# Kernel optimization log

Measured on AMD Instinct MI355X. Metric: run time of the kernel, lower is better.

Reference implementation:

```python
import jax, jax.numpy as jnp
import numpy as np

NEG_SLOPE = 0.2  # PyG GATConv default negative_slope


def _segment_softmax(alpha, dst, n):
    m = jax.ops.segment_max(alpha, dst, num_segments=n)
    m = jnp.where(jnp.isfinite(m), m, 0.0)
    ex = jnp.exp(alpha - m[dst])
    den = jax.ops.segment_sum(ex, dst, num_segments=n)
    return ex / (den[dst] + 1e-16)


def _gat_layer(x, src, dst, eattr, W, att_src, att_dst, We, att_e, b, n):
    h = x @ W                                        # [N, C]
    a = (h @ att_src)[src] + (h @ att_dst)[dst] + (eattr @ We) @ att_e  # [E]
    a = jax.nn.leaky_relu(a, NEG_SLOPE)
    coef = _segment_softmax(a, dst, n)               # edge-wise attention
    out = jax.ops.segment_sum(coef[:, None] * h[src], dst, num_segments=n)
    return out + b


def _glorot(key, shape):
    fan_in, fan_out = shape[0], shape[-1]
    s = jnp.sqrt(6.0 / (fan_in + fan_out))
    return jax.random.uniform(key, shape, jnp.float32, -s, s)


def setup_inputs() -> dict:
    N, E, D, ED = 100000, 1600000, 128, 16
    key = jax.random.key(0)
    ks = jax.random.split(key, 32)
    inp = {
        'x': jax.random.normal(ks[0], (N, D), jnp.float32),
        'edge_index': jax.random.randint(ks[1], (2, E), 0, N, jnp.int64),
        'edge_attr': jax.random.normal(ks[2], (E, ED), jnp.float32),
    }
    dims = [(D, 64), (64, 32), (32, 16)]
    i = 3
    for li, (din, dout) in enumerate(dims, 1):
        inp[f'W{li}'] = _glorot(ks[i], (din, dout)); i += 1
        inp[f'att_src{li}'] = _glorot(ks[i], (dout,)); i += 1
        inp[f'att_dst{li}'] = _glorot(ks[i], (dout,)); i += 1
        inp[f'We{li}'] = _glorot(ks[i], (ED, dout)); i += 1
        inp[f'att_e{li}'] = _glorot(ks[i], (dout,)); i += 1
        inp[f'b{li}'] = jnp.zeros((dout,), jnp.float32)
    return inp


def reference(x, edge_index, edge_attr,
              W1, att_src1, att_dst1, We1, att_e1, b1,
              W2, att_src2, att_dst2, We2, att_e2, b2,
              W3, att_src3, att_dst3, We3, att_e3, b3):
    n = x.shape[0]
    src, dst = edge_index[0], edge_index[1]
    # add self-loops; self-loop edge_attr = mean of incoming edge attrs (fill_value='mean')
    cnt = jax.ops.segment_sum(jnp.ones_like(dst, dtype=edge_attr.dtype), dst, num_segments=n)
    loop_attr = jax.ops.segment_sum(edge_attr, dst, num_segments=n) / jnp.maximum(cnt, 1.0)[:, None]
    loops = jnp.arange(n, dtype=src.dtype)
    src2 = jnp.concatenate([src, loops])
    dst2 = jnp.concatenate([dst, loops])
    ea2 = jnp.concatenate([edge_attr, loop_attr], axis=0)

    h = jax.nn.elu(_gat_layer(x, src2, dst2, ea2, W1, att_src1, att_dst1, We1, att_e1, b1, n))
    h = jax.nn.elu(_gat_layer(h, src2, dst2, ea2, W2, att_src2, att_dst2, We2, att_e2, b2, n))
    z = _gat_layer(h, src2, dst2, ea2, W3, att_src3, att_dst3, We3, att_e3, b3, n)
    return z
```

## Files before the change

### kernel.cpp

```cpp
#include <hip/hip_runtime.h>
#include <hip/hip_bf16.h>

typedef __hip_bfloat16 bf16;

__device__ __forceinline__ float lrelu(float a) { return a > 0.f ? a : 0.2f * a; }
__device__ __forceinline__ int clampi(int v, int hi) { return v < 0 ? 0 : (v >= hi ? hi - 1 : v); }
__device__ __forceinline__ float ldx(const void* p, size_t i, int f32) {
  return f32 ? ((const float*)p)[i] : (float)((const bf16*)p)[i];
}
__device__ __forceinline__ float4 ldx4(const void* p, size_t i, int f32) {
  if (f32) return *(const float4*)((const float*)p + i);
  const __hip_bfloat162* q = (const __hip_bfloat162*)((const bf16*)p + i);
  float2 a = __bfloat1622float2(q[0]), b = __bfloat1622float2(q[1]);
  return make_float4(a.x, a.y, b.x, b.y);
}

__device__ __forceinline__ void edge_qs(const void* eattr, size_t e, int f32, const float* w,
                                        float& q1, float& q2, float& q3) {
  float v[16];
  if (f32) {
    const float4* p = (const float4*)((const float*)eattr + e * 16);
#pragma unroll
    for (int j = 0; j < 4; ++j) {
      float4 t = p[j];
      v[4 * j] = t.x; v[4 * j + 1] = t.y; v[4 * j + 2] = t.z; v[4 * j + 3] = t.w;
    }
  } else {
    const __hip_bfloat162* p = (const __hip_bfloat162*)((const bf16*)eattr + e * 16);
#pragma unroll
    for (int j = 0; j < 8; ++j) {
      float2 t = __bfloat1622float2(p[j]);
      v[2 * j] = t.x; v[2 * j + 1] = t.y;
    }
  }
  q1 = 0.f; q2 = 0.f; q3 = 0.f;
#pragma unroll
  for (int j = 0; j < 16; ++j) {
    q1 += v[j] * w[j];
    q2 += v[j] * w[16 + j];
    q3 += v[j] * w[32 + j];
  }
}

__global__ __launch_bounds__(256) void detwv_k(const int* __restrict__ ei32,
                                               const unsigned short* __restrict__ xw, int E,
                                               int* __restrict__ flags, const void* We1,
                                               const void* ae1, const void* We2, const void* ae2,
                                               const void* We3, const void* ae3,
                                               float* __restrict__ wv) {
  __shared__ int s64, sf;
  int t = threadIdx.x;
  if (t == 0) { s64 = 1; sf = 0; }
  __syncthreads();
  int lim = E < 2048 ? E : 2048;
  for (int k = t; k < lim; k += 256)
    if (ei32[2 * k + 1] != 0) atomicAnd(&s64, 0);
  int hit = 0;
  for (int k = t; k < 4096; k += 256) {
    int ex = (xw[k] >> 7) & 0xFF;
    if (ex >= 0xC3) hit = 1;
  }
  if (hit) atomicOr(&sf, 1);
  __syncthreads();
  if (t == 0) { flags[0] = s64; flags[1] = sf; }
  int f32 = sf;
  if (t < 48) {
    int l = t >> 4, j = t & 15;
    const void* We = l == 0 ? We1 : (l == 1 ? We2 : We3);
    const void* ae = l == 0 ? ae1 : (l == 1 ? ae2 : ae3);
    int Cc = l == 0 ? 64 : (l == 1 ? 32 : 16);
    float s = 0.f;
    for (int c = 0; c < Cc; ++c) s += ldx(We, (size_t)j * Cc + c, f32) * ldx(ae, c, f32);
    wv[l * 16 + j] = s;
  }
}

__global__ __launch_bounds__(256) void count_k(const int* __restrict__ ei32, int E, int N,
                                               const int* __restrict__ flags,
                                               int* __restrict__ cnt, int* __restrict__ rank) {
  int e = blockIdx.x * 256 + threadIdx.x;
  if (e >= E) return;
  int is64 = flags[0] != 0;
  int d = is64 ? ei32[2 * ((size_t)E + e)] : ei32[(size_t)E + e];
  rank[e] = atomicAdd(&cnt[clampi(d, N)], 1);
}

__global__ __launch_bounds__(1024) void scan1_k(const int* __restrict__ cnt, int* __restrict__ excl,
                                                int* __restrict__ bsum, int n) {
  __shared__ int sh[1024];
  int i = blockIdx.x * 1024 + threadIdx.x;
  int v = (i < n) ? cnt[i] : 0;
  sh[threadIdx.x] = v;
  __syncthreads();
  for (int off = 1; off < 1024; off <<= 1) {
    int t = (threadIdx.x >= off) ? sh[threadIdx.x - off] : 0;
    __syncthreads();
    sh[threadIdx.x] += t;
    __syncthreads();
  }
  if (i < n) excl[i] = sh[threadIdx.x] - v;
  if (threadIdx.x == 1023) bsum[blockIdx.x] = sh[1023];
}

__global__ __launch_bounds__(128) void scan2_k(int* bsum, int nb) {
  __shared__ int sh[128];
  int t = threadIdx.x;
  int v = (t < nb) ? bsum[t] : 0;
  sh[t] = v;
  __syncthreads();
  for (int off = 1; off < 128; off <<= 1) {
    int x = (t >= off) ? sh[t - off] : 0;
    __syncthreads();
    sh[t] += x;
    __syncthreads();
  }
  if (t < nb) bsum[t] = sh[t] - v;
}

template <bool FOLD>
__global__ __launch_bounds__(256) void scan3_k(int* __restrict__ row_ptr,
                                               const int* __restrict__ bsum, int n, int E,
                                               int nb) {
  __shared__ int pref[128];
  int t = threadIdx.x;
  if (FOLD) {
    if (t < 128) pref[t] = (t < nb) ? bsum[t] : 0;
    __syncthreads();
    for (int off = 1; off < 128; off <<= 1) {
      int x = 0;
      if (t < 128 && t >= off) x = pref[t - off];
      __syncthreads();
      if (t < 128) pref[t] += x;
      __syncthreads();
    }
  }
  int i = blockIdx.x * 256 + t;
  if (i < n) {
    int blk = i >> 10;
    int add = FOLD ? (blk == 0 ? 0 : pref[blk - 1]) : bsum[blk];
    row_ptr[i] = row_ptr[i] + add;
  }
  if (i == 0) row_ptr[n] = E;
}

__global__ __launch_bounds__(256) void scatter_k(const int* __restrict__ ei32, const void* eattr,
                                                 const float* __restrict__ wv,
                                                 const int* __restrict__ flags,
                                                 const int* __restrict__ row_ptr,
                                                 const int* __restrict__ rank,
                                                 float4* __restrict__ recs, int E, int N) {
  __shared__ float w[48];
  if (threadIdx.x < 48) w[threadIdx.x] = wv[threadIdx.x];
  __syncthreads();
  int e = blockIdx.x * 256 + threadIdx.x;
  if (e >= E) return;
  int is64 = flags[0] != 0, f32 = flags[1] != 0;
  int s = is64 ? ei32[2 * (size_t)e] : ei32[e];
  int d = is64 ? ei32[2 * ((size_t)E + e)] : ei32[(size_t)E + e];
  s = clampi(s, N);
  d = clampi(d, N);
  int rk = rank[e];
  int base = row_ptr[d];
  float q1, q2, q3;
  edge_qs(eattr, (size_t)e, f32, w, q1, q2, q3);
  recs[clampi(base + rk, E)] = make_float4(__int_as_float(s), q1, q2, q3);
}

template <int K, int C, bool XEXT>
__global__ __launch_bounds__(256, 4) void mm3_k(const void* Xv, const void* Wv, const void* ats_v,
                                                const void* atd_v, const int* __restrict__ flags,
                                                int N, float* __restrict__ h,
                                                float* __restrict__ as_, float* __restrict__ ad_) {
  static_assert(K == 2 * C, "");
  constexpr int NCG = C / 8;
  constexpr int TM = 512 / NCG;
  __shared__ __align__(16) float Wl[K * C];
  __shared__ __align__(16) float Xl[32 * TM];
  const int f32 = flags[1];
  const int tid = threadIdx.x;
  for (int i = tid; i < K * C; i += 256) Wl[i] = ldx(Wv, i, f32);
  const int cg = tid & (NCG - 1);
  const int ng = tid / NCG;
  const int c0 = cg * 8;
  float ats[8], atd[8];
#pragma unroll
  for (int j = 0; j < 8; ++j) {
    ats[j] = ldx(ats_v, c0 + j, f32);
    atd[j] = ldx(atd_v, c0 + j, f32);
  }
  const int n_base = blockIdx.x * TM;
  float acc[2][8];
#pragma unroll
  for (int i = 0; i < 2; ++i)
#pragma unroll
    for (int j = 0; j < 8; ++j) acc[i][j] = 0.f;

#pragma unroll 1
  for (int kc = 0; kc < K / 32; ++kc) {
    __syncthreads();
#pragma unroll
    for (int t = 0; t < TM / 32; ++t) {
      int f = tid + t * 256;
      int node = f >> 3, kq = f & 7;
      int gn = n_base + node;
      if (gn >= N) gn = N - 1;
      float4 v;
      if (XEXT)
        v = ldx4(Xv, (size_t)gn * K + kc * 32 + kq * 4, f32);
      else
        v = *(const float4*)((const float*)Xv + (size_t)gn * K + kc * 32 + kq * 4);
      int col = node ^ (kq * 4);
      Xl[(kq * 4 + 0) * TM + col] = v.x;
      Xl[(kq * 4 + 1) * TM + col] = v.y;
      Xl[(kq * 4 + 2) * TM + col] = v.z;
      Xl[(kq * 4 + 3) * TM + col] = v.w;
    }
    __syncthreads();
#pragma unroll 8
    for (int kk = 0; kk < 32; ++kk) {
      const float2 xv = *(const float2*)&Xl[kk * TM + ((2 * ng) ^ ((kk >> 2) * 4))];
      const float4 w0 = *(const float4*)&Wl[(kc * 32 + kk) * C + c0];
      const float4 w1 = *(const float4*)&Wl[(kc * 32 + kk) * C + c0 + 4];
      const float ws[8] = {w0.x, w0.y, w0.z, w0.w, w1.x, w1.y, w1.z, w1.w};
#pragma unroll
      for (int j = 0; j < 8; ++j) {
        acc[0][j] += xv.x * ws[j];
        acc[1][j] += xv.y * ws[j];
      }
    }
  }
#pragma unroll
  for (int i = 0; i < 2; ++i) {
    int n = n_base + ng * 2 + i;
    float vs = 0.f, vd = 0.f;
#pragma unroll
    for (int j = 0; j < 8; ++j) {
      vs += acc[i][j] * ats[j];
      vd += acc[i][j] * atd[j];
    }
#pragma unroll
    for (int off = NCG / 2; off > 0; off >>= 1) {
      vs += __shfl_xor(vs, off, NCG);
      vd += __shfl_xor(vd, off, NCG);
    }
    if (n < N) {
      float* hr = &h[(size_t)n * C + c0];
      *(float4*)hr = make_float4(acc[i][0], acc[i][1], acc[i][2], acc[i][3]);
      *(float4*)(hr + 4) = make_float4(acc[i][4], acc[i][5], acc[i][6], acc[i][7]);
      if (cg == 0) {
        as_[n] = vs;
        ad_[n] = vd;
      }
    }
  }
}

template <int C, int QC, bool ELU, bool LAST>
__global__ __launch_bounds__(256) void agg_k(const int* __restrict__ row_ptr,
                                             const float4* __restrict__ recs,
                                             const float* __restrict__ as_,
                                             const float* __restrict__ ad_,
                                             const float* __restrict__ h, const void* b,
                                             const int* __restrict__ flags, void* out, int N,
                                             int E) {
  const int GR = 256 / C;
  constexpr int LP = C / 4;
  const float SHIFT = 10.0f;
  __shared__ int ss[256];
  __shared__ float sp[256];
  int lane = threadIdx.x & (C - 1);
  int grp = threadIdx.x / C;
  int slot0 = grp * C;
  int qtr = lane / LP;
  int lh = lane % LP;
  int f32 = flags[1];
  float bc = ldx(b, lane, f32);
  for (int n = blockIdx.x * GR + grp; n < N; n += gridDim.x * GR) {
    int start = row_ptr[n], end = row_ptr[n + 1];
    int deg = end > start ? end - start : 0;
    float adn = ad_[n];
    float denl = 0.f, qacc = 0.f;
    float4 a4 = make_float4(0.f, 0.f, 0.f, 0.f);
    for (int base = 0; base < deg; base += C) {
      int cnt = deg - base < C ? deg - base : C;
      int sj = 0;
      float pj = 0.f, qv = 0.f;
      if (lane < cnt) {
        float4 r = recs[start + base + lane];
        sj = clampi(__float_as_int(r.x), N);
        qv = ((const float*)&r)[QC];
        float aj = lrelu(as_[sj] + adn + qv);
        pj = __expf(aj - SHIFT);
      }
      qacc += qv;
      denl += pj;
      ss[slot0 + lane] = sj;
      sp[slot0 + lane] = pj;
      float4 s4 = make_float4(0.f, 0.f, 0.f, 0.f);
      int nt = (cnt + 3) >> 2;
#pragma unroll 4
      for (int t = 0; t < nt; ++t) {
        int r = t * 4 + qtr;
        int s = ss[slot0 + r];
        float p = sp[slot0 + r];
        const float4 hv = *(const float4*)&h[(size_t)s * C + 4 * lh];
        s4.x += p * hv.x;
        s4.y += p * hv.y;
        s4.z += p * hv.z;
        s4.w += p * hv.w;
      }
      a4.x += s4.x;
      a4.y += s4.y;
      a4.z += s4.z;
      a4.w += s4.w;
    }
    float den = denl, qsum = qacc;
#pragma unroll
    for (int off = C / 2; off > 0; off >>= 1) {
      den += __shfl_xor(den, off, C);
      qsum += __shfl_xor(qsum, off, C);
    }
    a4.x += __shfl_xor(a4.x, LP, C);
    a4.y += __shfl_xor(a4.y, LP, C);
    a4.z += __shfl_xor(a4.z, LP, C);
    a4.w += __shfl_xor(a4.w, LP, C);
    a4.x += __shfl_xor(a4.x, 2 * LP, C);
    a4.y += __shfl_xor(a4.y, 2 * LP, C);
    a4.z += __shfl_xor(a4.z, 2 * LP, C);
    a4.w += __shfl_xor(a4.w, 2 * LP, C);
    int ml = lane >> 2, bsel = lane & 3;
    float vx = __shfl(a4.x, ml, C);
    float vy = __shfl(a4.y, ml, C);
    float vz = __shfl(a4.z, ml, C);
    float vw = __shfl(a4.w, ml, C);
    float acc = bsel == 0 ? vx : (bsel == 1 ? vy : (bsel == 2 ? vz : vw));
    float qloop = qsum / fmaxf((float)deg, 1.0f);
    float aself = lrelu(as_[n] + adn + qloop);
    float pself = __expf(aself - SHIFT);
    den += pself;
    acc += pself * h[(size_t)n * C + lane];
    float o = acc / den + bc;
    if (ELU) o = o > 0.f ? o : (__expf(o) - 1.0f);
    if (LAST && !f32)
      ((bf16*)out)[(size_t)n * C + lane] = (bf16)o;
    else
      ((float*)out)[(size_t)n * C + lane] = o;
  }
}

extern "C" void kernel_launch(void* const* d_in, const int* in_sizes, int n_in, void* d_out,
                              int out_size, void* d_ws, size_t ws_size, hipStream_t stream) {
  const void* x = d_in[0];
  const int* ei32 = (const int*)d_in[1];
  void* eattr = d_in[2];
  const void *W1 = d_in[3], *s1 = d_in[4], *t1 = d_in[5], *We1 = d_in[6], *ae1 = d_in[7],
             *b1 = d_in[8];
  const void *W2 = d_in[9], *s2 = d_in[10], *t2 = d_in[11], *We2 = d_in[12], *ae2 = d_in[13],
             *b2 = d_in[14];
  const void *W3 = d_in[15], *s3 = d_in[16], *t3 = d_in[17], *We3 = d_in[18], *ae3 = d_in[19],
             *b3 = d_in[20];

  const int N = in_sizes[0] / 128;
  const int E = in_sizes[1] / 2;

  char* p = (char*)d_ws;
  auto alloc = [&](size_t bytes) -> void* {
    void* r = (void*)p;
    p += (bytes + 255) & ~(size_t)255;
    return r;
  };
  int* row_ptr = (int*)alloc((size_t)(N + 1) * 4);
  float4* recs = (float4*)alloc((size_t)E * 16);
  int* cnt = (int*)alloc((size_t)N * 4);
  int* rank = (int*)alloc((size_t)E * 4);
  int* bsum = (int*)alloc(128 * 4);
  float* wv = (float*)alloc(64 * 4);
  int* flags = (int*)alloc(256);
  float* as_ = (float*)alloc((size_t)N * 4);
  float* ad_ = (float*)alloc((size_t)N * 4);
  size_t used = (size_t)(p - (char*)d_ws);
  size_t need = 2 * ((size_t)N * 64 * 4 + 256);
  float *bufH, *bufO;
  if (used + need <= ws_size) {
    bufH = (float*)alloc((size_t)N * 64 * 4);
    bufO = (float*)alloc((size_t)N * 64 * 4);
  } else {
    bufH = (float*)eattr;
    bufO = (float*)eattr + (size_t)N * 64;
  }

  hipMemsetAsync(cnt, 0, (size_t)N * 4, stream);
  detwv_k<<<1, 256, 0, stream>>>(ei32, (const unsigned short*)x, E, flags, We1, ae1, We2, ae2, We3,
                                 ae3, wv);
  count_k<<<(E + 255) / 256, 256, 0, stream>>>(ei32, E, N, flags, cnt, rank);
  int nb = (N + 1023) / 1024;
  scan1_k<<<nb, 1024, 0, stream>>>(cnt, row_ptr, bsum, N);
  if (nb <= 128) {
    scan3_k<true><<<(N + 255) / 256, 256, 0, stream>>>(row_ptr, bsum, N, E, nb);
  } else {
    scan2_k<<<1, 128, 0, stream>>>(bsum, nb);
    scan3_k<false><<<(N + 255) / 256, 256, 0, stream>>>(row_ptr, bsum, N, E, nb);
  }
  scatter_k<<<(E + 255) / 256, 256, 0, stream>>>(ei32, eattr, wv, flags, row_ptr, rank, recs, E,
                                                 N);

  mm3_k<128, 64, true><<<(N + 63) / 64, 256, 0, stream>>>(x, W1, s1, t1, flags, N, bufH, as_, ad_);
  agg_k<64, 1, true, false><<<(N + 3) / 4, 256, 0, stream>>>(row_ptr, recs, as_, ad_, bufH, b1,
                                                             flags, bufO, N, E);
  mm3_k<64, 32, false><<<(N + 127) / 128, 256, 0, stream>>>(bufO, W2, s2, t2, flags, N, bufH, as_,
                                                            ad_);
  agg_k<32, 2, true, false><<<(N + 7) / 8, 256, 0, stream>>>(row_ptr, recs, as_, ad_, bufH, b2,
                                                             flags, bufO, N, E);
  mm3_k<32, 16, false><<<(N + 255) / 256, 256, 0, stream>>>(bufO, W3, s3, t3, flags, N, bufH, as_,
                                                            ad_);
  agg_k<16, 3, false, true><<<(N + 15) / 16, 256, 0, stream>>>(row_ptr, recs, as_, ad_, bufH, b3,
                                                               flags, d_out, N, E);
}
```

Baseline: 543.5 us.

## Precompute layer-1 attention weights and denominators in the edge scatter kernel

```diff
diff --git a/kernel.cpp b/kernel.cpp
--- a/kernel.cpp
+++ b/kernel.cpp
@@ -2,6 +2,8 @@
 #include <hip/hip_bf16.h>
 
 typedef __hip_bfloat16 bf16;
+
+constexpr float ASHIFT = 10.0f;
 
 __device__ __forceinline__ float lrelu(float a) { return a > 0.f ? a : 0.2f * a; }
 __device__ __forceinline__ int clampi(int v, int hi) { return v < 0 ? 0 : (v >= hi ? hi - 1 : v); }
@@ -143,11 +145,16 @@
   if (i == 0) row_ptr[n] = E;
 }
 
+template <bool PRE>
 __global__ __launch_bounds__(256) void scatter_k(const int* __restrict__ ei32, const void* eattr,
                                                  const float* __restrict__ wv,
                                                  const int* __restrict__ flags,
                                                  const int* __restrict__ row_ptr,
                                                  const int* __restrict__ rank,
+                                                 const float* __restrict__ as1,
+                                                 const float* __restrict__ ad1,
+                                                 float* __restrict__ qs1,
+                                                 float* __restrict__ den1,
                                                  float4* __restrict__ recs, int E, int N) {
   __shared__ float w[48];
   if (threadIdx.x < 48) w[threadIdx.x] = wv[threadIdx.x];
@@ -163,7 +170,15 @@
   int base = row_ptr[d];
   float q1, q2, q3;
   edge_qs(eattr, (size_t)e, f32, w, q1, q2, q3);
-  recs[clampi(base + rk, E)] = make_float4(__int_as_float(s), q1, q2, q3);
+  float y = q1;
+  if (PRE) {
+    float a1 = lrelu(as1[s] + ad1[d] + q1);
+    float p1 = __expf(a1 - ASHIFT);
+    atomicAdd(&qs1[d], q1);
+    atomicAdd(&den1[d], p1);
+    y = p1;
+  }
+  recs[clampi(base + rk, E)] = make_float4(__int_as_float(s), y, q2, q3);
 }
 
 template <int K, int C, bool XEXT>
@@ -255,17 +270,18 @@
   }
 }
 
-template <int C, int QC, bool ELU, bool LAST>
+template <int C, int QC, bool ELU, bool LAST, bool PRE>
 __global__ __launch_bounds__(256) void agg_k(const int* __restrict__ row_ptr,
                                              const float4* __restrict__ recs,
                                              const float* __restrict__ as_,
                                              const float* __restrict__ ad_,
+                                             const float* __restrict__ qsp,
+                                             const float* __restrict__ denp,
                                              const float* __restrict__ h, const void* b,
                                              const int* __restrict__ flags, void* out, int N,
                                              int E) {
   const int GR = 256 / C;
   constexpr int LP = C / 4;
-  const float SHIFT = 10.0f;
   __shared__ int ss[256];
   __shared__ float sp[256];
   int lane = threadIdx.x & (C - 1);
@@ -284,16 +300,25 @@
     for (int base = 0; base < deg; base += C) {
       int cnt = deg - base < C ? deg - base : C;
       int sj = 0;
-      float pj = 0.f, qv = 0.f;
-      if (lane < cnt) {
-        float4 r = recs[start + base + lane];
-        sj = clampi(__float_as_int(r.x), N);
-        qv = ((const float*)&r)[QC];
-        float aj = lrelu(as_[sj] + adn + qv);
-        pj = __expf(aj - SHIFT);
+      float pj = 0.f;
+      if (PRE) {
+        if (lane < cnt) {
+          float4 r = recs[start + base + lane];
+          sj = clampi(__float_as_int(r.x), N);
+          pj = r.y;
+        }
+      } else {
+        float qv = 0.f;
+        if (lane < cnt) {
+          float4 r = recs[start + base + lane];
+          sj = clampi(__float_as_int(r.x), N);
+          qv = ((const float*)&r)[QC];
+          float aj = lrelu(as_[sj] + adn + qv);
+          pj = __expf(aj - ASHIFT);
+        }
+        qacc += qv;
+        denl += pj;
       }
-      qacc += qv;
-      denl += pj;
       ss[slot0 + lane] = sj;
       sp[slot0 + lane] = pj;
       float4 s4 = make_float4(0.f, 0.f, 0.f, 0.f);
@@ -314,11 +339,18 @@
       a4.z += s4.z;
       a4.w += s4.w;
     }
-    float den = denl, qsum = qacc;
-#pragma unroll
-    for (int off = C / 2; off > 0; off >>= 1) {
-      den += __shfl_xor(den, off, C);
-      qsum += __shfl_xor(qsum, off, C);
+    float den, qsum;
+    if (PRE) {
+      den = denp[n];
+      qsum = qsp[n];
+    } else {
+      den = denl;
+      qsum = qacc;
+#pragma unroll
+      for (int off = C / 2; off > 0; off >>= 1) {
+        den += __shfl_xor(den, off, C);
+        qsum += __shfl_xor(qsum, off, C);
+      }
     }
     a4.x += __shfl_xor(a4.x, LP, C);
     a4.y += __shfl_xor(a4.y, LP, C);
@@ -336,7 +368,7 @@
     float acc = bsel == 0 ? vx : (bsel == 1 ? vy : (bsel == 2 ? vz : vw));
     float qloop = qsum / fmaxf((float)deg, 1.0f);
     float aself = lrelu(as_[n] + adn + qloop);
-    float pself = __expf(aself - SHIFT);
+    float pself = __expf(aself - ASHIFT);
     den += pself;
     acc += pself * h[(size_t)n * C + lane];
     float o = acc / den + bc;
@@ -378,10 +410,13 @@
   int* flags = (int*)alloc(256);
   float* as_ = (float*)alloc((size_t)N * 4);
   float* ad_ = (float*)alloc((size_t)N * 4);
+  float* qs1 = (float*)alloc((size_t)N * 4);
+  float* den1 = (float*)alloc((size_t)N * 4);
   size_t used = (size_t)(p - (char*)d_ws);
   size_t need = 2 * ((size_t)N * 64 * 4 + 256);
   float *bufH, *bufO;
-  if (used + need <= ws_size) {
+  bool hasbuf = used + need <= ws_size;
+  if (hasbuf) {
     bufH = (float*)alloc((size_t)N * 64 * 4);
     bufO = (float*)alloc((size_t)N * 64 * 4);
   } else {
@@ -401,18 +436,30 @@
     scan2_k<<<1, 128, 0, stream>>>(bsum, nb);
     scan3_k<false><<<(N + 255) / 256, 256, 0, stream>>>(row_ptr, bsum, N, E, nb);
   }
-  scatter_k<<<(E + 255) / 256, 256, 0, stream>>>(ei32, eattr, wv, flags, row_ptr, rank, recs, E,
-                                                 N);
-
-  mm3_k<128, 64, true><<<(N + 63) / 64, 256, 0, stream>>>(x, W1, s1, t1, flags, N, bufH, as_, ad_);
-  agg_k<64, 1, true, false><<<(N + 3) / 4, 256, 0, stream>>>(row_ptr, recs, as_, ad_, bufH, b1,
-                                                             flags, bufO, N, E);
+
+  if (hasbuf) {
+    hipMemsetAsync(qs1, 0, (size_t)N * 4, stream);
+    hipMemsetAsync(den1, 0, (size_t)N * 4, stream);
+    mm3_k<128, 64, true><<<(N + 63) / 64, 256, 0, stream>>>(x, W1, s1, t1, flags, N, bufH, as_,
+                                                            ad_);
+    scatter_k<true><<<(E + 255) / 256, 256, 0, stream>>>(ei32, eattr, wv, flags, row_ptr, rank,
+                                                         as_, ad_, qs1, den1, recs, E, N);
+    agg_k<64, 1, true, false, true><<<(N + 3) / 4, 256, 0, stream>>>(
+        row_ptr, recs, as_, ad_, qs1, den1, bufH, b1, flags, bufO, N, E);
+  } else {
+    scatter_k<false><<<(E + 255) / 256, 256, 0, stream>>>(ei32, eattr, wv, flags, row_ptr, rank,
+                                                          as_, ad_, qs1, den1, recs, E, N);
+    mm3_k<128, 64, true><<<(N + 63) / 64, 256, 0, stream>>>(x, W1, s1, t1, flags, N, bufH, as_,
+                                                            ad_);
+    agg_k<64, 1, true, false, false><<<(N + 3) / 4, 256, 0, stream>>>(
+        row_ptr, recs, as_, ad_, qs1, den1, bufH, b1, flags, bufO, N, E);
+  }
   mm3_k<64, 32, false><<<(N + 127) / 128, 256, 0, stream>>>(bufO, W2, s2, t2, flags, N, bufH, as_,
                                                             ad_);
-  agg_k<32, 2, true, false><<<(N + 7) / 8, 256, 0, stream>>>(row_ptr, recs, as_, ad_, bufH, b2,
-                                                             flags, bufO, N, E);
+  agg_k<32, 2, true, false, false><<<(N + 7) / 8, 256, 0, stream>>>(
+      row_ptr, recs, as_, ad_, qs1, den1, bufH, b2, flags, bufO, N, E);
   mm3_k<32, 16, false><<<(N + 255) / 256, 256, 0, stream>>>(bufO, W3, s3, t3, flags, N, bufH, as_,
                                                             ad_);
-  agg_k<16, 3, false, true><<<(N + 15) / 16, 256, 0, stream>>>(row_ptr, recs, as_, ad_, bufH, b3,
-                                                               flags, d_out, N, E);
-}
+  agg_k<16, 3, false, true, false><<<(N + 15) / 16, 256, 0, stream>>>(
+      row_ptr, recs, as_, ad_, qs1, den1, bufH, b3, flags, d_out, N, E);
+}
```

Measured after the change: 647.4 us. 1.19x slower.
